# Performance work log

Hardware: AMD Instinct MI355X
Metric: run time of the kernel (lower is better)

The kernel has to match this reference:

```python
import jax, jax.numpy as jnp
import numpy as np

# Production GravNet config: 8 events x 4096 hits, K=40 neighbours, 4 spatial dims
B, V, K, S, P, F_IN, F_OUT = 8, 4096, 40, 4, 64, 64, 128
N = B * V
MAX_RADIUS_SQ = 1.0  # SelectKnn(max_radius=1.0)


def setup_inputs() -> dict:
    key = jax.random.key(0)
    ks = jax.random.split(key, 7)
    x = jax.random.normal(ks[0], (N, F_IN), jnp.float32)
    # Dense layer params (glorot-ish scaling)
    W_prop = jax.random.normal(ks[1], (F_IN, P), jnp.float32) / np.sqrt(F_IN)
    b_prop = jnp.zeros((P,), jnp.float32)
    W_sp = jax.random.normal(ks[2], (F_IN, S), jnp.float32) / np.sqrt(F_IN)
    b_sp = jnp.zeros((S,), jnp.float32)
    # output transform input dim = n_prop_total (2*P) + F_IN
    W_out = jax.random.normal(ks[3], (2 * P + F_IN, F_OUT), jnp.float32) / np.sqrt(2 * P + F_IN)
    b_out = jnp.zeros((F_OUT,), jnp.float32)
    row_splits = jnp.arange(B + 1, dtype=jnp.int32) * V  # equal-size ragged segments
    return dict(x=x, W_prop=W_prop, b_prop=b_prop, W_sp=W_sp, b_sp=b_sp,
                W_out=W_out, b_out=b_out, row_splits=row_splits)


def _knn_indices(coords):
    """Per-event brute-force KNN. coords: [N,S] -> global neighbour idx [N,K]."""
    c = coords.reshape(B, V, S)
    # pairwise squared distances within each event: [B,V,V]
    d = jnp.sum((c[:, :, None, :] - c[:, None, :, :]) ** 2, axis=-1)
    neg_d, idx = jax.lax.top_k(-d, K + 1)  # nearest first; col 0 is self (d=0)
    idx, dsq = idx[:, :, 1:], -neg_d[:, :, 1:]
    # tf_compatible max_radius: out-of-radius neighbours -> self index
    self_idx = jnp.arange(V, dtype=idx.dtype)[None, :, None]
    idx = jnp.where(dsq > MAX_RADIUS_SQ, self_idx, idx)
    gidx = idx + (jnp.arange(B, dtype=idx.dtype) * V)[:, None, None]
    return gidx.reshape(N, K)


def reference(x, W_prop, b_prop, W_sp, b_sp, W_out, b_out, row_splits):
    coords = x @ W_sp + b_sp                      # [N,S] learned coordinates
    nidx = _knn_indices(coords)                   # [N,K] (int, non-diff)
    nb_coords = coords[nidx]                      # [N,K,S] gather
    dsq = jnp.sum((coords[:, None, :] - nb_coords) ** 2, axis=-1)  # [N,K]
    feat = x @ W_prop + b_prop                    # [N,P]
    w = jnp.exp(-10.0 * dsq)[:, :, None]          # gauss_of_lin(10*d^2)
    nf = feat[nidx] * w                           # [N,K,P]
    agg = jnp.concatenate([nf.max(axis=1), nf.mean(axis=1)], axis=-1)  # [N,2P]
    out = jnp.tanh(jnp.concatenate([agg, x], axis=-1) @ W_out + b_out)  # [N,F_OUT]
    return out
```

## Files before the change

### kernel.cpp

```cpp
#include <hip/hip_runtime.h>
#include <cstdint>
#include <cstddef>

#define NB   8
#define VV   4096
#define KNN  40
#define NTOT 32768
#define CAP  224
#define INFB 0x7F800000u
#define ONEB 0x3F800000u

__device__ __forceinline__ int xbucket(float x) {
  int b = (int)floorf((x + 4.f) * 32.f);
  return b < 0 ? 0 : (b > 255 ? 255 : b);
}

__global__ __launch_bounds__(256) void k_prep(
    const float* __restrict__ x, const float* __restrict__ W_prop,
    const float* __restrict__ b_prop, const float* __restrict__ W_sp,
    const float* __restrict__ b_sp, const float* __restrict__ W_out,
    float* __restrict__ coords, float* __restrict__ feat,
    float* __restrict__ xW)
{
  __shared__ float xt[64][64];
  const int t = threadIdx.x;
  const int row0 = blockIdx.x * 64;

  #pragma unroll
  for (int i = 0; i < 16; ++i) {
    int idx = t + i * 256;
    xt[idx >> 6][idx & 63] = x[(size_t)row0 * 64 + idx];
  }
  __syncthreads();

  {
    const int col = t & 63, rb = (t >> 6) * 16;
    float acc[16];
    #pragma unroll
    for (int i = 0; i < 16; ++i) acc[i] = b_prop[col];
    for (int k = 0; k < 64; k += 4) {
      const float w0 = W_prop[(k + 0) * 64 + col];
      const float w1 = W_prop[(k + 1) * 64 + col];
      const float w2 = W_prop[(k + 2) * 64 + col];
      const float w3 = W_prop[(k + 3) * 64 + col];
      #pragma unroll
      for (int i = 0; i < 16; ++i) {
        const float4 a4 = *(const float4*)&xt[rb + i][k];
        acc[i] += a4.x * w0 + a4.y * w1 + a4.z * w2 + a4.w * w3;
      }
    }
    #pragma unroll
    for (int i = 0; i < 16; ++i)
      feat[(size_t)(row0 + rb + i) * 64 + col] = acc[i];
  }

  {
    const int col = t & 127, who = t >> 7;
    #pragma unroll
    for (int p = 0; p < 2; ++p) {
      const int rb = who * 16 + p * 32;
      float acc[16];
      #pragma unroll
      for (int i = 0; i < 16; ++i) acc[i] = 0.f;
      for (int k = 0; k < 64; k += 4) {
        const float w0 = W_out[(size_t)(128 + k + 0) * 128 + col];
        const float w1 = W_out[(size_t)(128 + k + 1) * 128 + col];
        const float w2 = W_out[(size_t)(128 + k + 2) * 128 + col];
        const float w3 = W_out[(size_t)(128 + k + 3) * 128 + col];
        #pragma unroll
        for (int i = 0; i < 16; ++i) {
          const float4 a4 = *(const float4*)&xt[rb + i][k];
          acc[i] += a4.x * w0 + a4.y * w1 + a4.z * w2 + a4.w * w3;
        }
      }
      #pragma unroll
      for (int i = 0; i < 16; ++i)
        xW[(size_t)(row0 + rb + i) * 128 + col] = acc[i];
    }
  }

  if (t < 64) {
    float a0 = b_sp[0], a1 = b_sp[1], a2 = b_sp[2], a3 = b_sp[3];
    for (int k = 0; k < 64; ++k) {
      const float xv = xt[t][k];
      a0 += xv * W_sp[k * 4 + 0];
      a1 += xv * W_sp[k * 4 + 1];
      a2 += xv * W_sp[k * 4 + 2];
      a3 += xv * W_sp[k * 4 + 3];
    }
    ((float4*)coords)[row0 + t] = make_float4(a0, a1, a2, a3);
  }
}

__global__ __launch_bounds__(512) void k_sort(
    float* __restrict__ coords, unsigned short* __restrict__ perm,
    unsigned short* __restrict__ prefg)
{
  __shared__ float4 cs[VV];
  __shared__ int hist[256];
  __shared__ int pref[257];
  const int t = threadIdx.x, ev = blockIdx.x;
  const int evbase = ev * VV;
  float4* cg = (float4*)coords + evbase;

  for (int i = t; i < VV; i += 512) cs[i] = cg[i];
  if (t < 256) hist[t] = 0;
  __syncthreads();

  for (int i = t; i < VV; i += 512)
    atomicAdd(&hist[xbucket(cs[i].x)], 1);
  __syncthreads();

  if (t < 64) {
    const int l = t;
    const int h0 = hist[4*l], h1 = hist[4*l+1], h2 = hist[4*l+2], h3 = hist[4*l+3];
    const int s = h0 + h1 + h2 + h3;
    int incl = s;
    #pragma unroll
    for (int off = 1; off < 64; off <<= 1) {
      const int v = __shfl_up(incl, off);
      if (l >= off) incl += v;
    }
    const int excl = incl - s;
    pref[4*l]   = excl;
    pref[4*l+1] = excl + h0;
    pref[4*l+2] = excl + h0 + h1;
    pref[4*l+3] = excl + h0 + h1 + h2;
    if (l == 63) pref[256] = excl + s;
  }
  __syncthreads();
  if (t < 256) hist[t] = 0;
  __syncthreads();

  for (int i = t; i < VV; i += 512) {
    const int b = xbucket(cs[i].x);
    const int pos = pref[b] + atomicAdd(&hist[b], 1);
    cg[pos] = cs[i];
    perm[evbase + pos] = (unsigned short)i;
  }
  if (t < 257) prefg[ev * 257 + t] = (unsigned short)pref[t];
}

template <int NC>
__device__ __forceinline__ unsigned bs40(const uint2* __restrict__ list,
                                         int M, int lane) {
  unsigned dv[NC];
  #pragma unroll
  for (int j = 0; j < NC; ++j) {
    const int e = lane + j * 64;
    dv[j] = (e < M) ? list[e].x : INFB;
  }
  unsigned lo = 0, hi = ONEB;
  while (lo < hi) {
    const unsigned mid = (lo + hi) >> 1;
    int cnt = 0;
    #pragma unroll
    for (int j = 0; j < NC; ++j)
      cnt += (int)__popcll(__ballot(dv[j] <= mid));
    if (cnt >= KNN) hi = mid; else lo = mid + 1;
  }
  return hi;
}

#define AGG_CHUNK(J0, N)                                                     \
  {                                                                          \
    float fv[N], wgt[N];                                                     \
    _Pragma("unroll")                                                        \
    for (int j = 0; j < N; ++j) {                                            \
      const uint2 en = list[(J0) + j];                                       \
      wgt[j] = __expf(-10.f * __uint_as_float(en.x));                        \
      const int ei = __builtin_amdgcn_readfirstlane((int)en.y);              \
      fv[j] = fe[(size_t)ei * 64 + lane];                                    \
    }                                                                        \
    _Pragma("unroll")                                                        \
    for (int j = 0; j < N; ++j) {                                            \
      const float v = fv[j] * wgt[j];                                        \
      vmax = fmaxf(vmax, v);                                                 \
      vsum += v;                                                             \
    }                                                                        \
  }

__global__ __launch_bounds__(512, 4) void k_knn(
    const float* __restrict__ coords,
    const unsigned short* __restrict__ perm,
    const unsigned short* __restrict__ prefg,
    const float* __restrict__ feat, float* __restrict__ agg)
{
  __shared__ float4 cs[VV];
  __shared__ uint2 lists[8][CAP];
  __shared__ unsigned short pr[257];

  const int t = threadIdx.x, lane = t & 63;
  const int wvid = __builtin_amdgcn_readfirstlane(t) >> 6;
  const int bid0 = blockIdx.x;
  const int bid = (bid0 & 7) * 64 + (bid0 >> 3);
  const int ev = bid >> 6;
  const int slot = bid & 63;
  const int evbase = ev * VV;

  {
    const float4* cg = (const float4*)coords + evbase;
    for (int i = t; i < VV; i += 512) cs[i] = cg[i];
    if (t < 257) pr[t] = prefg[ev * 257 + t];
  }
  __syncthreads();

  uint2* list = lists[wvid];
  const float* fe = feat + (size_t)evbase * 64;
  const unsigned long long lmask = (1ull << lane) - 1ull;

  auto scan = [&](unsigned rbits, int q, float4 qc, int lo, int hi) -> int {
    int M = 0;
    #pragma unroll 4
    for (int base = lo; base < hi; base += 64) {
      const int c = base + lane;
      const float4 cc = cs[c];
      const float dx = qc.x - cc.x, dy = qc.y - cc.y;
      const float dz = qc.z - cc.z, dw = qc.w - cc.w;
      const float dsq = dx * dx + dy * dy + dz * dz + dw * dw;
      const bool pred = (__float_as_uint(dsq) <= rbits) && (c != q);
      const unsigned long long bm = __ballot(pred);
      if (pred) {
        const int pos = M + (int)__popcll(bm & lmask);
        if (pos < CAP)
          list[pos] = make_uint2(__float_as_uint(dsq), (unsigned)c);
      }
      M += (int)__popcll(bm);
    }
    return M;
  };

  for (int qi = 0; qi < 8; ++qi) {
    const int q = slot + (qi * 8 + wvid) * 64;
    const float4 qc = cs[q];
    const int origq = (int)perm[evbase + q];
    const int bq = xbucket(qc.x);
    const int wlo = ((int)pr[bq > 32 ? bq - 32 : 0]) & ~63;
    const int whi0 = (int)pr[bq + 33 > 256 ? 256 : bq + 33];
    const int whi = (whi0 + 63) & ~63;

    int M = scan(ONEB, q, qc, wlo, whi);
    bool ok = true;

    if (M > CAP) {
      const unsigned t0 = bs40<4>(list, CAP, lane);
      M = scan(t0, q, qc, wlo, whi);
      ok = (M <= CAP);
    }

    float vmax = -__builtin_inff(), vsum = 0.f;

    if (ok) {
      for (int be = 0; be < M; be += 64) {
        const int e = be + lane;
        if (e < M) {
          uint2 en = list[e];
          en.y = (unsigned)perm[evbase + (int)en.y];
          list[e] = en;
        }
      }

      int Msel;
      if (M > KNN) {
        unsigned taub;
        if      (M <=  64) taub = bs40<1>(list, M, lane);
        else if (M <= 128) taub = bs40<2>(list, M, lane);
        else               taub = bs40<4>(list, M, lane);
        int S = 0;
        for (int be = 0; be < M; be += 64) {
          const int e = be + lane;
          uint2 en = make_uint2(0u, 0u);
          bool p = false;
          if (e < M) { en = list[e]; p = (en.x <= taub); }
          const unsigned long long bm = __ballot(p);
          if (p) list[S + (int)__popcll(bm & lmask)] = en;
          S += (int)__popcll(bm);
        }
        Msel = S;
      } else {
        if (lane >= M && lane < KNN)
          list[lane] = make_uint2(0u, (unsigned)origq);
        Msel = KNN;
      }

      if (Msel == KNN) {
        AGG_CHUNK(0, 16)
        AGG_CHUNK(16, 16)
        AGG_CHUNK(32, 8)
      } else {
        #pragma unroll 4
        for (int e = 0; e < Msel; ++e) {
          const uint2 en = list[e];
          const int ei = __builtin_amdgcn_readfirstlane((int)en.y);
          const float w = __expf(-10.f * __uint_as_float(en.x));
          const float v = fe[(size_t)ei * 64 + lane] * w;
          vmax = fmaxf(vmax, v);
          vsum += v;
        }
      }
    } else {
      unsigned lo = 0, hi = ONEB;
      while (lo < hi) {
        const unsigned mid = (lo + hi) >> 1;
        const float fm = __uint_as_float(mid);
        int cnt = 0;
        for (int base = wlo; base < whi; base += 64) {
          const int c = base + lane;
          const float4 cc = cs[c];
          const float dx = qc.x - cc.x, dy = qc.y - cc.y;
          const float dz = qc.z - cc.z, dw = qc.w - cc.w;
          const float dsq = dx * dx + dy * dy + dz * dz + dw * dw;
          cnt += (int)__popcll(__ballot(dsq <= fm && c != q));
        }
        if (cnt >= KNN) hi = mid; else lo = mid + 1;
      }
      const float tau = __uint_as_float(hi);
      for (int c = wlo; c < whi; ++c) {
        if (c == q) continue;
        const float4 cc = cs[c];
        const float dx = qc.x - cc.x, dy = qc.y - cc.y;
        const float dz = qc.z - cc.z, dw = qc.w - cc.w;
        const float dsq = dx * dx + dy * dy + dz * dz + dw * dw;
        if (dsq <= tau) {
          const int ei = (int)perm[evbase + c];
          const float w = __expf(-10.f * dsq);
          const float v = fe[(size_t)ei * 64 + lane] * w;
          vmax = fmaxf(vmax, v);
          vsum += v;
        }
      }
    }

    const int g = evbase + origq;
    agg[(size_t)g * 128 + lane]      = vmax;
    agg[(size_t)g * 128 + 64 + lane] = vsum * (1.f / 40.f);
  }
}

__global__ __launch_bounds__(256) void k_out(
    const float* __restrict__ agg, const float* __restrict__ W_out,
    const float* __restrict__ b_out, float* __restrict__ out)
{
  __shared__ float at[64][128];
  const int t = threadIdx.x;
  const int row0 = blockIdx.x * 64;

  #pragma unroll
  for (int i = 0; i < 32; ++i) {
    int idx = t + i * 256;
    at[idx >> 7][idx & 127] = agg[(size_t)row0 * 128 + idx];
  }
  __syncthreads();

  const int col = t & 127, who = t >> 7;
  #pragma unroll
  for (int p = 0; p < 2; ++p) {
    const int rb = who * 16 + p * 32;
    float acc[16];
    #pragma unroll
    for (int i = 0; i < 16; ++i) acc[i] = 0.f;
    for (int k = 0; k < 128; k += 4) {
      const float w0 = W_out[(size_t)(k + 0) * 128 + col];
      const float w1 = W_out[(size_t)(k + 1) * 128 + col];
      const float w2 = W_out[(size_t)(k + 2) * 128 + col];
      const float w3 = W_out[(size_t)(k + 3) * 128 + col];
      #pragma unroll
      for (int i = 0; i < 16; ++i) {
        const float4 a4 = *(const float4*)&at[rb + i][k];
        acc[i] += a4.x * w0 + a4.y * w1 + a4.z * w2 + a4.w * w3;
      }
    }
    const float bb = b_out[col];
    #pragma unroll
    for (int i = 0; i < 16; ++i) {
      const size_t o = (size_t)(row0 + rb + i) * 128 + col;
      float v = acc[i] + bb + out[o];
      v = fminf(15.f, fmaxf(-15.f, v));
      const float e = __expf(2.f * v);
      out[o] = (e - 1.f) / (e + 1.f);
    }
  }
}

extern "C" void kernel_launch(void* const* d_in, const int* in_sizes, int n_in,
                              void* d_out, int out_size, void* d_ws, size_t ws_size,
                              hipStream_t stream) {
  const float* x      = (const float*)d_in[0];
  const float* W_prop = (const float*)d_in[1];
  const float* b_prop = (const float*)d_in[2];
  const float* W_sp   = (const float*)d_in[3];
  const float* b_sp   = (const float*)d_in[4];
  const float* W_out  = (const float*)d_in[5];
  const float* b_out  = (const float*)d_in[6];

  float* out = (float*)d_out;
  char* ws = (char*)d_ws;
  float* coords          = (float*)ws;
  float* feat            = (float*)(ws + (512 << 10));
  float* agg             = (float*)(ws + (512 << 10) + (8 << 20));
  unsigned short* perm   = (unsigned short*)(ws + (512 << 10) + (24 << 20));
  unsigned short* prefg  = (unsigned short*)(ws + (512 << 10) + (24 << 20) + (64 << 10));

  k_prep<<<NTOT / 64, 256, 0, stream>>>(x, W_prop, b_prop, W_sp, b_sp, W_out,
                                        coords, feat, out );
  k_sort<<<NB, 512, 0, stream>>>(coords, perm, prefg);
  k_knn<<<NB * (VV / 64), 512, 0, stream>>>(coords, perm, prefg, feat, agg);
  k_out<<<NTOT / 64, 256, 0, stream>>>(agg, W_out, b_out, out);
}
```

Measured before the change: 177.2 us.

## Split per-event sort into global histogram, prefix and scatter; double KNN grid

The single-block-per-event counting sort is replaced by three steps: histogram atomics fused into the prep kernel, a one-block prefix kernel, and a scatter kernel spread over 64 blocks. The 8-block serial sort was a bottleneck. The KNN grid is doubled so each block handles 4 queries per wave instead of 8. The radius bisection becomes a ternary search that does two ballots per step. The costs are more launches, a memset, and global atomics, and the scatter order inside a bucket is now nondeterministic.

```diff
diff --git a/kernel.cpp b/kernel.cpp
--- a/kernel.cpp
+++ b/kernel.cpp
@@ -20,7 +20,7 @@
     const float* __restrict__ b_prop, const float* __restrict__ W_sp,
     const float* __restrict__ b_sp, const float* __restrict__ W_out,
     float* __restrict__ coords, float* __restrict__ feat,
-    float* __restrict__ xW)
+    float* __restrict__ xW, int* __restrict__ hist)
 {
   __shared__ float xt[64][64];
   const int t = threadIdx.x;
@@ -89,56 +89,50 @@
       a3 += xv * W_sp[k * 4 + 3];
     }
     ((float4*)coords)[row0 + t] = make_float4(a0, a1, a2, a3);
-  }
-}
-
-__global__ __launch_bounds__(512) void k_sort(
-    float* __restrict__ coords, unsigned short* __restrict__ perm,
-    unsigned short* __restrict__ prefg)
+    const int ev = (row0 + t) >> 12;
+    atomicAdd(&hist[ev * 256 + xbucket(a0)], 1);
+  }
+}
+
+__global__ __launch_bounds__(512) void k_prefix(
+    const int* __restrict__ hist, unsigned short* __restrict__ prefg,
+    int* __restrict__ cursor)
 {
-  __shared__ float4 cs[VV];
-  __shared__ int hist[256];
-  __shared__ int pref[257];
-  const int t = threadIdx.x, ev = blockIdx.x;
+  const int t = threadIdx.x, w = t >> 6, l = t & 63;
+  const int* h = hist + w * 256;
+  const int h0 = h[4*l], h1 = h[4*l+1], h2 = h[4*l+2], h3 = h[4*l+3];
+  const int s = h0 + h1 + h2 + h3;
+  int incl = s;
+  #pragma unroll
+  for (int off = 1; off < 64; off <<= 1) {
+    const int v = __shfl_up(incl, off);
+    if (l >= off) incl += v;
+  }
+  const int excl = incl - s;
+  const int p0 = excl, p1 = excl + h0, p2 = excl + h0 + h1, p3 = excl + h0 + h1 + h2;
+  prefg[w * 257 + 4*l]     = (unsigned short)p0;
+  prefg[w * 257 + 4*l + 1] = (unsigned short)p1;
+  prefg[w * 257 + 4*l + 2] = (unsigned short)p2;
+  prefg[w * 257 + 4*l + 3] = (unsigned short)p3;
+  cursor[w * 256 + 4*l]     = p0;
+  cursor[w * 256 + 4*l + 1] = p1;
+  cursor[w * 256 + 4*l + 2] = p2;
+  cursor[w * 256 + 4*l + 3] = p3;
+  if (l == 63) prefg[w * 257 + 256] = (unsigned short)(excl + s);
+}
+
+__global__ __launch_bounds__(512) void k_scatter(
+    const float* __restrict__ coords, float* __restrict__ csort,
+    unsigned short* __restrict__ perm, int* __restrict__ cursor)
+{
+  const int ev = blockIdx.x >> 3;
+  const int i = ((blockIdx.x & 7) << 9) + threadIdx.x;
   const int evbase = ev * VV;
-  float4* cg = (float4*)coords + evbase;
-
-  for (int i = t; i < VV; i += 512) cs[i] = cg[i];
-  if (t < 256) hist[t] = 0;
-  __syncthreads();
-
-  for (int i = t; i < VV; i += 512)
-    atomicAdd(&hist[xbucket(cs[i].x)], 1);
-  __syncthreads();
-
-  if (t < 64) {
-    const int l = t;
-    const int h0 = hist[4*l], h1 = hist[4*l+1], h2 = hist[4*l+2], h3 = hist[4*l+3];
-    const int s = h0 + h1 + h2 + h3;
-    int incl = s;
-    #pragma unroll
-    for (int off = 1; off < 64; off <<= 1) {
-      const int v = __shfl_up(incl, off);
-      if (l >= off) incl += v;
-    }
-    const int excl = incl - s;
-    pref[4*l]   = excl;
-    pref[4*l+1] = excl + h0;
-    pref[4*l+2] = excl + h0 + h1;
-    pref[4*l+3] = excl + h0 + h1 + h2;
-    if (l == 63) pref[256] = excl + s;
-  }
-  __syncthreads();
-  if (t < 256) hist[t] = 0;
-  __syncthreads();
-
-  for (int i = t; i < VV; i += 512) {
-    const int b = xbucket(cs[i].x);
-    const int pos = pref[b] + atomicAdd(&hist[b], 1);
-    cg[pos] = cs[i];
-    perm[evbase + pos] = (unsigned short)i;
-  }
-  if (t < 257) prefg[ev * 257 + t] = (unsigned short)pref[t];
+  const float4 c = ((const float4*)coords)[evbase + i];
+  const int b = xbucket(c.x);
+  const int pos = atomicAdd(&cursor[ev * 256 + b], 1);
+  ((float4*)csort)[evbase + pos] = c;
+  perm[evbase + pos] = (unsigned short)i;
 }
 
 template <int NC>
@@ -152,12 +146,18 @@
   }
   unsigned lo = 0, hi = ONEB;
   while (lo < hi) {
-    const unsigned mid = (lo + hi) >> 1;
-    int cnt = 0;
-    #pragma unroll
-    for (int j = 0; j < NC; ++j)
-      cnt += (int)__popcll(__ballot(dv[j] <= mid));
-    if (cnt >= KNN) hi = mid; else lo = mid + 1;
+    const unsigned span = hi - lo;
+    const unsigned m1 = lo + span / 3;
+    const unsigned m2 = lo + (span - span / 3);
+    int c1 = 0, c2 = 0;
+    #pragma unroll
+    for (int j = 0; j < NC; ++j) {
+      c1 += (int)__popcll(__ballot(dv[j] <= m1));
+      c2 += (int)__popcll(__ballot(dv[j] <= m2));
+    }
+    if (c1 >= KNN)      hi = m1;
+    else if (c2 >= KNN) { lo = m1 + 1; hi = m2; }
+    else                lo = m2 + 1;
   }
   return hi;
 }
@@ -174,7 +174,7 @@
     }                                                                        \
     _Pragma("unroll")                                                        \
     for (int j = 0; j < N; ++j) {                                            \
-      const float v = fv[j] * wgt[j];                                        \
+      const float v = fv[j] * wgt[j];                                       \
       vmax = fmaxf(vmax, v);                                                 \
       vsum += v;                                                             \
     }                                                                        \
@@ -193,9 +193,9 @@
   const int t = threadIdx.x, lane = t & 63;
   const int wvid = __builtin_amdgcn_readfirstlane(t) >> 6;
   const int bid0 = blockIdx.x;
-  const int bid = (bid0 & 7) * 64 + (bid0 >> 3);
-  const int ev = bid >> 6;
-  const int slot = bid & 63;
+  const int bid = (bid0 & 7) * 128 + (bid0 >> 3);
+  const int ev = bid >> 7;
+  const int slot = bid & 127;
   const int evbase = ev * VV;
 
   {
@@ -230,8 +230,8 @@
     return M;
   };
 
-  for (int qi = 0; qi < 8; ++qi) {
-    const int q = slot + (qi * 8 + wvid) * 64;
+  for (int qi = 0; qi < 4; ++qi) {
+    const int q = slot + (qi * 8 + wvid) * 128;
     const float4 qc = cs[q];
     const int origq = (int)perm[evbase + q];
     const int bq = xbucket(qc.x);
@@ -395,15 +395,21 @@
 
   float* out = (float*)d_out;
   char* ws = (char*)d_ws;
-  float* coords          = (float*)ws;
-  float* feat            = (float*)(ws + (512 << 10));
-  float* agg             = (float*)(ws + (512 << 10) + (8 << 20));
-  unsigned short* perm   = (unsigned short*)(ws + (512 << 10) + (24 << 20));
-  unsigned short* prefg  = (unsigned short*)(ws + (512 << 10) + (24 << 20) + (64 << 10));
-
+  float* coords          = (float*)(ws);
+  float* csort           = (float*)(ws + (512 << 10));
+  float* feat            = (float*)(ws + (1 << 20));
+  float* agg             = (float*)(ws + (9 << 20));
+  unsigned short* perm   = (unsigned short*)(ws + (25 << 20));
+  unsigned short* prefg  = (unsigned short*)(ws + (25 << 20) + 65536);
+  int* hist              = (int*)(ws + (25 << 20) + 65536 + 4608);
+  int* cursor            = (int*)(ws + (25 << 20) + 65536 + 4608 + 8192);
+
+  hipMemsetAsync(hist, 0, 8192, stream);
   k_prep<<<NTOT / 64, 256, 0, stream>>>(x, W_prop, b_prop, W_sp, b_sp, W_out,
-                                        coords, feat, out );
-  k_sort<<<NB, 512, 0, stream>>>(coords, perm, prefg);
-  k_knn<<<NB * (VV / 64), 512, 0, stream>>>(coords, perm, prefg, feat, agg);
+                                        coords, feat, out ,
+                                        hist);
+  k_prefix<<<1, 512, 0, stream>>>(hist, prefg, cursor);
+  k_scatter<<<NB * 8, 512, 0, stream>>>(coords, csort, perm, cursor);
+  k_knn<<<NB * (VV / 32), 512, 0, stream>>>(csort, perm, prefg, feat, agg);
   k_out<<<NTOT / 64, 256, 0, stream>>>(agg, W_out, b_out, out);
 }
```

Result: slower. 204.0 us (+15.1%).
